# Optimization experiments

Hardware: AMD Instinct MI355X
Metric: run time of the kernel (lower is better)

Reference implementation:

```python
import jax, jax.numpy as jnp
from jax import lax
import numpy as np

TWO_PI = 2.0 * np.pi

# ---- batched real-amplitude statevector simulator (RY/CNOT only -> real state) ----

def _init_state(batch, n):
    s = jnp.zeros((batch, 2 ** n), dtype=jnp.float32).at[:, 0].set(1.0)
    return s.reshape((batch,) + (2,) * n)

def _ry(state, wire, theta, n):
    # state: (B, 2,...,2); theta: scalar or (B,)
    ax = wire + 1
    h = theta * 0.5
    c = jnp.reshape(jnp.cos(h), (-1,) + (1,) * (n - 1))
    s = jnp.reshape(jnp.sin(h), (-1,) + (1,) * (n - 1))
    s0 = lax.index_in_dim(state, 0, ax, keepdims=False)
    s1 = lax.index_in_dim(state, 1, ax, keepdims=False)
    return jnp.stack([c * s0 - s * s1, s * s0 + c * s1], axis=ax)

def _cnot(state, ctrl, tgt):
    axc, axt = ctrl + 1, tgt + 1
    s0 = lax.index_in_dim(state, 0, axc, keepdims=True)
    s1 = lax.index_in_dim(state, 1, axc, keepdims=True)
    return jnp.concatenate([s0, jnp.flip(s1, axis=axt)], axis=axc)

def _expz(state, wire, n):
    sgn = jnp.reshape(jnp.array([1.0, -1.0], state.dtype),
                      (1,) * (wire + 1) + (2,) + (1,) * (n - wire - 1))
    return jnp.sum(state * state * sgn, axis=tuple(range(1, n + 1)))

# gate lists: ('ry', theta_index, wire) or ('cx', control, target)
EDGE_OPS = [('ry',0,0),('ry',1,1),('cx',0,1),('ry',2,2),('ry',3,3),('cx',3,2),
            ('ry',4,4),('ry',5,5),('cx',4,5),('ry',6,6),('ry',7,7),('cx',7,6),
            ('ry',8,1),('ry',9,2),('cx',1,2),('ry',10,5),('ry',11,6),('cx',6,5),
            ('ry',12,2),('ry',13,5),('cx',2,5),('ry',14,5)]

NODE_OPS = [('ry',0,0),('ry',1,1),('cx',0,1),('ry',2,2),('ry',3,3),('cx',3,2),
            ('ry',4,4),('ry',5,5),('cx',4,5),('ry',6,6),('ry',7,7),('cx',7,6),
            ('ry',8,8),('ry',9,9),('cx',8,9),('ry',10,10),('ry',11,11),('cx',11,10),
            ('ry',12,1),('ry',13,2),('cx',1,2),('ry',14,5),('ry',15,6),('cx',6,5),
            ('ry',16,9),('ry',17,10),('cx',10,9),('ry',18,2),('ry',19,5),('cx',2,5),
            ('ry',20,5),('ry',21,9),('cx',5,9),('ry',22,4)]

def _circuit(angles, theta, ops, n, meas_wire):
    st = _init_state(angles.shape[0], n)
    for i in range(n):  # input encoding RYs, per-sample angles
        st = _ry(st, i, angles[:, i], n)
    for op in ops:
        if op[0] == 'ry':
            st = _ry(st, op[2], theta[op[1]], n)
        else:
            st = _cnot(st, op[1], op[2])
    return _expz(st, meas_wire, n)

# ---- GNN pieces ----

def _edge_net(H, Ri, Ro, theta):
    bo = Ro.T @ H                      # [E,4]
    bi = Ri.T @ H                      # [E,4]
    B = jnp.concatenate([bo, bi], axis=1)  # [E,8]
    return (1.0 - _circuit(B, theta, EDGE_OPS, 8, 5)) * 0.5

def _node_net(H, e, Ri, Ro, theta):
    bo = Ro.T @ H                      # [E,4]
    bi = Ri.T @ H                      # [E,4]
    mi = (Ri * e[None, :]) @ bo        # [N,4]
    mo = (Ro * e[None, :]) @ bi        # [N,4]
    M = jnp.concatenate([mi, mo, H], axis=1)  # [N,12]
    return jnp.pi * (1.0 - _circuit(M, theta, NODE_OPS, 12, 9))

def _gnn(X, Ri, Ro, W_in, b_in, theta_edge, theta_node, n_iters=2):
    H = jnp.concatenate([jax.nn.sigmoid(X @ W_in + b_in) * TWO_PI, X], axis=1)  # [N,4]
    e = _edge_net(H, Ri, Ro, theta_edge)
    for _ in range(n_iters):
        h = _node_net(H, e, Ri, Ro, theta_node)   # [N]
        H = jnp.concatenate([h[:, None], X], axis=1)
        e = _edge_net(H, Ri, Ro, theta_edge)
    return e


def setup_inputs() -> dict:
    key = jax.random.key(0)
    ks = jax.random.split(key, 6)
    N, E = 2048, 4096
    X = jax.random.normal(ks[0], (N, 3), jnp.float32)
    recv = jax.random.randint(ks[1], (E,), 0, N)
    send = jax.random.randint(ks[2], (E,), 0, N)
    cols = jnp.arange(E)
    Ri = jnp.zeros((N, E), jnp.float32).at[recv, cols].set(1.0)
    Ro = jnp.zeros((N, E), jnp.float32).at[send, cols].set(1.0)
    W_in = jax.random.normal(ks[3], (3, 1), jnp.float32)
    b_in = jnp.zeros((1,), jnp.float32)
    theta_edge = jax.random.uniform(ks[4], (15,), jnp.float32, 0.0, TWO_PI)
    theta_node = jax.random.uniform(ks[5], (23,), jnp.float32, 0.0, TWO_PI)
    return {'X': X, 'Ri': Ri, 'Ro': Ro, 'W_in': W_in, 'b_in': b_in,
            'theta_edge': theta_edge, 'theta_node': theta_node}


def reference(X, Ri, Ro, W_in, b_in, theta_edge, theta_node):
    return _gnn(X, Ri, Ro, W_in, b_in, theta_edge, theta_node, n_iters=2)
```

## Files before the change

kernel.cpp:

```cpp
#include <hip/hip_runtime.h>
#include <math.h>

#define N_NODES 2048
#define N_EDGES 4096
#define PI_F 3.14159265358979323846f
#define TWO_PI_F 6.28318530717958647692f

#define NBLK 256
#define NTHR 256
#define NSCAN (NBLK * NTHR)
#define TOT4 (N_NODES * N_EDGES / 4)

__device__ __forceinline__ float agent_load(const float* p) {
    return __hip_atomic_load(p, __ATOMIC_RELAXED, __HIP_MEMORY_SCOPE_AGENT);
}
__device__ __forceinline__ int agent_load_i(const int* p) {
    return __hip_atomic_load(p, __ATOMIC_RELAXED, __HIP_MEMORY_SCOPE_AGENT);
}
__device__ __forceinline__ void agent_store_i(int* p, int v) {
    __hip_atomic_store(p, v, __ATOMIC_RELAXED, __HIP_MEMORY_SCOPE_AGENT);
}
__device__ __forceinline__ void spin_ge(const int* p, int v) {
    while (__hip_atomic_load(p, __ATOMIC_RELAXED, __HIP_MEMORY_SCOPE_AGENT) < v)
        __builtin_amdgcn_s_sleep(2);
    asm volatile("" ::: "memory");
}


template<int M>
__device__ __forceinline__ void ry16(float* a, float c, float s) {
#pragma unroll
    for (int i = 0; i < 16; ++i)
        if (!(i & M)) {
            int j = i | M;
            float x0 = a[i], x1 = a[j];
            a[i] = c * x0 - s * x1;
            a[j] = s * x0 + c * x1;
        }
}
template<int MC, int MT>
__device__ __forceinline__ void cx16(float* a) {
#pragma unroll
    for (int i = 0; i < 16; ++i)
        if ((i & MC) && !(i & MT)) {
            int j = i | MT;
            float t = a[i]; a[i] = a[j]; a[j] = t;
        }
}

template<bool BTYPE>
__device__ __forceinline__ void sub16(const float* ic, const float* is,
                                      const float* thc, const float* ths,
                                      float& z, float& x) {
    float a[16];
    a[0] = ic[3]; a[1] = is[3];
#pragma unroll
    for (int i = 0; i < 2; ++i) { a[i | 2] = a[i] * is[2]; a[i] *= ic[2]; }
#pragma unroll
    for (int i = 0; i < 4; ++i) { a[i | 4] = a[i] * is[1]; a[i] *= ic[1]; }
#pragma unroll
    for (int i = 0; i < 8; ++i) { a[i | 8] = a[i] * is[0]; a[i] *= ic[0]; }
    ry16<8>(a, thc[0], ths[0]);
    ry16<4>(a, thc[1], ths[1]);
    cx16<8, 4>(a);
    ry16<2>(a, thc[2], ths[2]);
    ry16<1>(a, thc[3], ths[3]);
    cx16<1, 2>(a);
    ry16<4>(a, thc[4], ths[4]);
    ry16<2>(a, thc[5], ths[5]);
    if (BTYPE) { cx16<2, 4>(a); ry16<4>(a, thc[6], ths[6]); }
    else       { cx16<4, 2>(a); ry16<2>(a, thc[6], ths[6]); }
    const int m = BTYPE ? 4 : 2;
    z = 0.f; x = 0.f;
#pragma unroll
    for (int i = 0; i < 16; ++i) z += (i & m) ? -a[i] * a[i] : a[i] * a[i];
    if (BTYPE) {
#pragma unroll
        for (int i = 0; i < 16; ++i) if (!(i & 4)) x += a[i] * a[i | 4];
        x *= 2.f;
    }
}

__device__ __forceinline__ float node_update(
        const float* M, float& chh, float& shh,
        const float* cxv, const float* sxv,
        const float* tnC, const float* tnS, float C20, float S20) {
    float zB9, dmy;
    {
        float ic[4] = {chh, cxv[0], cxv[1], cxv[2]};
        float is[4] = {shh, sxv[0], sxv[1], sxv[2]};
        float thc[7] = {tnC[8],tnC[9],tnC[10],tnC[11],tnC[16],tnC[17],tnC[21]};
        float ths[7] = {tnS[8],tnS[9],tnS[10],tnS[11],tnS[16],tnS[17],tnS[21]};
        sub16<true>(ic, is, thc, ths, zB9, dmy);
    }
    float mC[8], mS[8];
#pragma unroll
    for (int k = 0; k < 8; ++k) __sincosf(0.5f * M[k], &mS[k], &mC[k]);
    float zA1, zA2, xA2;
    {
        float thc[7] = {tnC[0],tnC[1],tnC[2],tnC[3],tnC[12],tnC[13],tnC[18]};
        float ths[7] = {tnS[0],tnS[1],tnS[2],tnS[3],tnS[12],tnS[13],tnS[18]};
        sub16<false>(&mC[0], &mS[0], thc, ths, zA1, dmy);
    }
    {
        float thc[7] = {tnC[4],tnC[5],tnC[6],tnC[7],tnC[14],tnC[15],tnC[19]};
        float ths[7] = {tnS[4],tnS[5],tnS[6],tnS[7],tnS[14],tnS[15],tnS[19]};
        sub16<true>(&mC[4], &mS[4], thc, ths, zA2, xA2);
    }
    float p9 = (C20*zA1*zA2 - S20*xA2) * zB9;
    float h = PI_F * (1.f - p9);
    __sincosf(0.5f*h, &shh, &chh);
    return h;
}

__device__ __forceinline__ void scatter8(float ev, const float4& Hs, const float4& Hr,
                                         int si, int ri,
                                         float* __restrict__ macc, int* __restrict__ arr) {
    atomicAdd(&macc[ri*8+0], ev*Hs.x); atomicAdd(&macc[ri*8+1], ev*Hs.y);
    atomicAdd(&macc[ri*8+2], ev*Hs.z); atomicAdd(&macc[ri*8+3], ev*Hs.w);
    atomicAdd(&macc[si*8+4], ev*Hr.x); atomicAdd(&macc[si*8+5], ev*Hr.y);
    atomicAdd(&macc[si*8+6], ev*Hr.z); atomicAdd(&macc[si*8+7], ev*Hr.w);
    asm volatile("s_waitcnt vmcnt(0)" ::: "memory");
    atomicAdd(&arr[ri], 1); atomicAdd(&arr[si], 1);
}

__global__ __launch_bounds__(256) void k_fused(
        const float* __restrict__ X, const float* __restrict__ Ri,
        const float* __restrict__ Ro, const float* __restrict__ W,
        const float* __restrict__ b, const float* __restrict__ te,
        const float* __restrict__ tn,
        int* __restrict__ send, int* __restrict__ recv,
        float* __restrict__ maccA, float* __restrict__ maccB,
        int* __restrict__ arrA, int* __restrict__ arrB,
        int* __restrict__ deg, int* __restrict__ sdone,
        float* __restrict__ out) {
    __shared__ float s_teC[16], s_teS[16], s_tnC[24], s_tnS[24];
    int blk = blockIdx.x, tid = threadIdx.x;
    bool edge_blk = (blk < 64);

    if (edge_blk) {
        if (tid < 14) {
            float s, c; __sincosf(0.5f * te[tid], &s, &c);
            s_teC[tid] = c; s_teS[tid] = s;
        } else if (tid == 14) {
            float s, c; __sincosf(te[14], &s, &c);
            s_teC[14] = c; s_teS[14] = s;
        } else if (tid < 15 + 22) {
            int k = tid - 15; float s, c;
            if (k == 20) __sincosf(tn[20], &s, &c);
            else         __sincosf(0.5f * tn[k], &s, &c);
            s_tnC[k] = c; s_tnS[k] = s;
        }
    }

    {
        int gid = blk * NTHR + tid;
        const float4* Ri4 = (const float4*)Ri;
        const float4* Ro4 = (const float4*)Ro;
#pragma unroll 1
        for (int t0 = gid; t0 < TOT4; t0 += 8 * NSCAN) {
            float4 vi[8], vo[8];
#pragma unroll
            for (int u = 0; u < 8; ++u) {
                int t = t0 + u * NSCAN;
                vi[u] = Ri4[t]; vo[u] = Ro4[t];
            }
#pragma unroll
            for (int u = 0; u < 8; ++u) {
                int t = t0 + u * NSCAN;
                int base = t * 4;
                int row = base >> 12;
                int e   = base & (N_EDGES - 1);
                int cnt = 0;
                if (vi[u].x != 0.f) { agent_store_i(recv+e+0, row+1); ++cnt; }
                if (vi[u].y != 0.f) { agent_store_i(recv+e+1, row+1); ++cnt; }
                if (vi[u].z != 0.f) { agent_store_i(recv+e+2, row+1); ++cnt; }
                if (vi[u].w != 0.f) { agent_store_i(recv+e+3, row+1); ++cnt; }
                if (vo[u].x != 0.f) { agent_store_i(send+e+0, row+1); ++cnt; }
                if (vo[u].y != 0.f) { agent_store_i(send+e+1, row+1); ++cnt; }
                if (vo[u].z != 0.f) { agent_store_i(send+e+2, row+1); ++cnt; }
                if (vo[u].w != 0.f) { agent_store_i(send+e+3, row+1); ++cnt; }
                if (cnt) atomicAdd(&deg[row], cnt);
            }
        }
        asm volatile("s_waitcnt vmcnt(0)" ::: "memory");
        __syncthreads();
        if (tid == 0) atomicAdd(sdone, 1);
    }
    if (!edge_blk || tid >= 64) return;

    int e = blk * 64 + tid;

    int si, ri;
    {
        int v;
        while ((v = agent_load_i(send + e)) == 0) __builtin_amdgcn_s_sleep(1);
        si = v - 1;
        while ((v = agent_load_i(recv + e)) == 0) __builtin_amdgcn_s_sleep(1);
        ri = v - 1;
        asm volatile("" ::: "memory");
    }

    float xs0 = X[si*3+0], xs1 = X[si*3+1], xs2 = X[si*3+2];
    float xr0 = X[ri*3+0], xr1 = X[ri*3+1], xr2 = X[ri*3+2];
    float w0 = W[0], w1 = W[1], w2 = W[2], bb = b[0];
    float hs = TWO_PI_F / (1.f + __expf(-(xs0*w0 + xs1*w1 + xs2*w2 + bb)));
    float hr = TWO_PI_F / (1.f + __expf(-(xr0*w0 + xr1*w1 + xr2*w2 + bb)));
    float chs, shs, chr, shr, cxs[3], sxs[3], cxr[3], sxr[3];
    __sincosf(0.5f*hs,  &shs,    &chs);
    __sincosf(0.5f*xs0, &sxs[0], &cxs[0]);
    __sincosf(0.5f*xs1, &sxs[1], &cxs[1]);
    __sincosf(0.5f*xs2, &sxs[2], &cxs[2]);
    __sincosf(0.5f*hr,  &shr,    &chr);
    __sincosf(0.5f*xr0, &sxr[0], &cxr[0]);
    __sincosf(0.5f*xr1, &sxr[1], &cxr[1]);
    __sincosf(0.5f*xr2, &sxr[2], &cxr[2]);
    float C14 = s_teC[14], S14 = s_teS[14];
    float C20 = s_tnC[20], S20 = s_tnS[20];

    float zA, zB, xB, dmy;
    {
        float ic[4] = {chs, cxs[0], cxs[1], cxs[2]};
        float is[4] = {shs, sxs[0], sxs[1], sxs[2]};
        float thc[7] = {s_teC[0],s_teC[1],s_teC[2],s_teC[3],s_teC[8],s_teC[9],s_teC[12]};
        float ths[7] = {s_teS[0],s_teS[1],s_teS[2],s_teS[3],s_teS[8],s_teS[9],s_teS[12]};
        sub16<false>(ic, is, thc, ths, zA, dmy);
    }
    {
        float ic[4] = {chr, cxr[0], cxr[1], cxr[2]};
        float is[4] = {shr, sxr[0], sxr[1], sxr[2]};
        float thc[7] = {s_teC[4],s_teC[5],s_teC[6],s_teC[7],s_teC[10],s_teC[11],s_teC[13]};
        float ths[7] = {s_teS[4],s_teS[5],s_teS[6],s_teS[7],s_teS[10],s_teS[11],s_teS[13]};
        sub16<true>(ic, is, thc, ths, zB, xB);
    }
    float ev = 0.5f*(1.f - (C14*zA*zB - S14*xB));
    scatter8(ev, make_float4(hs, xs0, xs1, xs2),
                 make_float4(hr, xr0, xr1, xr2), si, ri, maccA, arrA);

    spin_ge(sdone, NBLK);
    int dgs = agent_load_i(deg + si);
    int dgr = agent_load_i(deg + ri);

#pragma unroll
    for (int it = 0; it < 2; ++it) {
        const float* mc_ = it ? maccB : maccA;
        const int*   ar  = it ? arrB  : arrA;
        while (agent_load_i(ar + si) < dgs || agent_load_i(ar + ri) < dgr)
            __builtin_amdgcn_s_sleep(1);
        asm volatile("" ::: "memory");
        float Ms[8], Mr[8];
#pragma unroll
        for (int k = 0; k < 8; ++k) Ms[k] = agent_load(mc_ + si*8 + k);
#pragma unroll
        for (int k = 0; k < 8; ++k) Mr[k] = agent_load(mc_ + ri*8 + k);
        hs = node_update(Ms, chs, shs, cxs, sxs, s_tnC, s_tnS, C20, S20);
        hr = node_update(Mr, chr, shr, cxr, sxr, s_tnC, s_tnS, C20, S20);
        {
            float ic[4] = {chs, cxs[0], cxs[1], cxs[2]};
            float is[4] = {shs, sxs[0], sxs[1], sxs[2]};
            float thc[7] = {s_teC[0],s_teC[1],s_teC[2],s_teC[3],s_teC[8],s_teC[9],s_teC[12]};
            float ths[7] = {s_teS[0],s_teS[1],s_teS[2],s_teS[3],s_teS[8],s_teS[9],s_teS[12]};
            sub16<false>(ic, is, thc, ths, zA, dmy);
        }
        {
            float ic[4] = {chr, cxr[0], cxr[1], cxr[2]};
            float is[4] = {shr, sxr[0], sxr[1], sxr[2]};
            float thc[7] = {s_teC[4],s_teC[5],s_teC[6],s_teC[7],s_teC[10],s_teC[11],s_teC[13]};
            float ths[7] = {s_teS[4],s_teS[5],s_teS[6],s_teS[7],s_teS[10],s_teS[11],s_teS[13]};
            sub16<true>(ic, is, thc, ths, zB, xB);
        }
        ev = 0.5f*(1.f - (C14*zA*zB - S14*xB));
        if (it == 0) {
            scatter8(ev, make_float4(hs, xs0, xs1, xs2),
                         make_float4(hr, xr0, xr1, xr2), si, ri, maccB, arrB);
        } else {
            out[e] = ev;
        }
    }
}

extern "C" void kernel_launch(void* const* d_in, const int* in_sizes, int n_in,
                              void* d_out, int out_size, void* d_ws, size_t ws_size,
                              hipStream_t stream) {
    const float* X  = (const float*)d_in[0];
    const float* Ri = (const float*)d_in[1];
    const float* Ro = (const float*)d_in[2];
    const float* W  = (const float*)d_in[3];
    const float* b  = (const float*)d_in[4];
    const float* te = (const float*)d_in[5];
    const float* tn = (const float*)d_in[6];
    float* out = (float*)d_out;

    int*   send  = (int*)d_ws;
    int*   recv  = send + N_EDGES;
    float* maccA = (float*)(recv + N_EDGES);
    float* maccB = maccA + N_NODES * 8;
    int*   arrA  = (int*)(maccB + N_NODES * 8);
    int*   arrB  = arrA + N_NODES;
    int*   deg   = arrB + N_NODES;
    int*   sdone = deg + N_NODES;
    size_t zbytes = (size_t)(2*N_EDGES + 2*N_NODES*8 + 3*N_NODES + 16) * 4;

    hipMemsetAsync((void*)send, 0, zbytes, stream);
    k_fused<<<NBLK, NTHR, 0, stream>>>(X, Ri, Ro, W, b, te, tn,
                                       send, recv, maccA, maccB,
                                       arrA, arrB, deg, sdone, out);
}
```

Baseline: 128.7 us.

## Split dense scan into separate kernel and drop inter-block spin flags

```diff
diff --git a/kernel.cpp b/kernel.cpp
--- a/kernel.cpp
+++ b/kernel.cpp
@@ -6,9 +6,9 @@
 #define PI_F 3.14159265358979323846f
 #define TWO_PI_F 6.28318530717958647692f
 
-#define NBLK 256
-#define NTHR 256
-#define NSCAN (NBLK * NTHR)
+#define SBLK 256
+#define STHR 256
+#define NSCAN (SBLK * STHR)
 #define TOT4 (N_NODES * N_EDGES / 4)
 
 __device__ __forceinline__ float agent_load(const float* p) {
@@ -16,14 +16,6 @@
 }
 __device__ __forceinline__ int agent_load_i(const int* p) {
     return __hip_atomic_load(p, __ATOMIC_RELAXED, __HIP_MEMORY_SCOPE_AGENT);
-}
-__device__ __forceinline__ void agent_store_i(int* p, int v) {
-    __hip_atomic_store(p, v, __ATOMIC_RELAXED, __HIP_MEMORY_SCOPE_AGENT);
-}
-__device__ __forceinline__ void spin_ge(const int* p, int v) {
-    while (__hip_atomic_load(p, __ATOMIC_RELAXED, __HIP_MEMORY_SCOPE_AGENT) < v)
-        __builtin_amdgcn_s_sleep(2);
-    asm volatile("" ::: "memory");
 }
 
 
@@ -81,125 +73,82 @@
     }
 }
 
-__device__ __forceinline__ float node_update(
-        const float* M, float& chh, float& shh,
-        const float* cxv, const float* sxv,
-        const float* tnC, const float* tnS, float C20, float S20) {
-    float zB9, dmy;
-    {
-        float ic[4] = {chh, cxv[0], cxv[1], cxv[2]};
-        float is[4] = {shh, sxv[0], sxv[1], sxv[2]};
-        float thc[7] = {tnC[8],tnC[9],tnC[10],tnC[11],tnC[16],tnC[17],tnC[21]};
-        float ths[7] = {tnS[8],tnS[9],tnS[10],tnS[11],tnS[16],tnS[17],tnS[21]};
-        sub16<true>(ic, is, thc, ths, zB9, dmy);
-    }
-    float mC[8], mS[8];
-#pragma unroll
-    for (int k = 0; k < 8; ++k) __sincosf(0.5f * M[k], &mS[k], &mC[k]);
-    float zA1, zA2, xA2;
-    {
-        float thc[7] = {tnC[0],tnC[1],tnC[2],tnC[3],tnC[12],tnC[13],tnC[18]};
-        float ths[7] = {tnS[0],tnS[1],tnS[2],tnS[3],tnS[12],tnS[13],tnS[18]};
-        sub16<false>(&mC[0], &mS[0], thc, ths, zA1, dmy);
-    }
-    {
-        float thc[7] = {tnC[4],tnC[5],tnC[6],tnC[7],tnC[14],tnC[15],tnC[19]};
-        float ths[7] = {tnS[4],tnS[5],tnS[6],tnS[7],tnS[14],tnS[15],tnS[19]};
-        sub16<true>(&mC[4], &mS[4], thc, ths, zA2, xA2);
-    }
-    float p9 = (C20*zA1*zA2 - S20*xA2) * zB9;
-    float h = PI_F * (1.f - p9);
-    __sincosf(0.5f*h, &shh, &chh);
-    return h;
-}
-
-__device__ __forceinline__ void scatter8(float ev, const float4& Hs, const float4& Hr,
+__global__ __launch_bounds__(256) void k_scan(
+        const float* __restrict__ Ri, const float* __restrict__ Ro,
+        int* __restrict__ send, int* __restrict__ recv, int* __restrict__ deg) {
+    int gid = blockIdx.x * STHR + threadIdx.x;
+    const float4* Ri4 = (const float4*)Ri;
+    const float4* Ro4 = (const float4*)Ro;
+#pragma unroll 1
+    for (int t0 = gid; t0 < TOT4; t0 += 8 * NSCAN) {
+        float4 vi[8], vo[8];
+#pragma unroll
+        for (int u = 0; u < 8; ++u) {
+            int t = t0 + u * NSCAN;
+            vi[u] = Ri4[t]; vo[u] = Ro4[t];
+        }
+#pragma unroll
+        for (int u = 0; u < 8; ++u) {
+            int t = t0 + u * NSCAN;
+            int base = t * 4;
+            int row = base >> 12;
+            int e   = base & (N_EDGES - 1);
+            int cnt = 0;
+            if (vi[u].x != 0.f) { recv[e+0] = row; ++cnt; }
+            if (vi[u].y != 0.f) { recv[e+1] = row; ++cnt; }
+            if (vi[u].z != 0.f) { recv[e+2] = row; ++cnt; }
+            if (vi[u].w != 0.f) { recv[e+3] = row; ++cnt; }
+            if (vo[u].x != 0.f) { send[e+0] = row; ++cnt; }
+            if (vo[u].y != 0.f) { send[e+1] = row; ++cnt; }
+            if (vo[u].z != 0.f) { send[e+2] = row; ++cnt; }
+            if (vo[u].w != 0.f) { send[e+3] = row; ++cnt; }
+            if (cnt) atomicAdd(&deg[row], cnt);
+        }
+    }
+}
+
+__device__ __forceinline__ void scatter8(float ev, float hs, float hr,
+                                         float xs0, float xs1, float xs2,
+                                         float xr0, float xr1, float xr2,
                                          int si, int ri,
                                          float* __restrict__ macc, int* __restrict__ arr) {
-    atomicAdd(&macc[ri*8+0], ev*Hs.x); atomicAdd(&macc[ri*8+1], ev*Hs.y);
-    atomicAdd(&macc[ri*8+2], ev*Hs.z); atomicAdd(&macc[ri*8+3], ev*Hs.w);
-    atomicAdd(&macc[si*8+4], ev*Hr.x); atomicAdd(&macc[si*8+5], ev*Hr.y);
-    atomicAdd(&macc[si*8+6], ev*Hr.z); atomicAdd(&macc[si*8+7], ev*Hr.w);
+    atomicAdd(&macc[ri*8+0], ev*hs);  atomicAdd(&macc[ri*8+1], ev*xs0);
+    atomicAdd(&macc[ri*8+2], ev*xs1); atomicAdd(&macc[ri*8+3], ev*xs2);
+    atomicAdd(&macc[si*8+4], ev*hr);  atomicAdd(&macc[si*8+5], ev*xr0);
+    atomicAdd(&macc[si*8+6], ev*xr1); atomicAdd(&macc[si*8+7], ev*xr2);
     asm volatile("s_waitcnt vmcnt(0)" ::: "memory");
     atomicAdd(&arr[ri], 1); atomicAdd(&arr[si], 1);
 }
 
-__global__ __launch_bounds__(256) void k_fused(
-        const float* __restrict__ X, const float* __restrict__ Ri,
-        const float* __restrict__ Ro, const float* __restrict__ W,
+__global__ __launch_bounds__(64) void k_mega(
+        const float* __restrict__ X, const float* __restrict__ W,
         const float* __restrict__ b, const float* __restrict__ te,
         const float* __restrict__ tn,
-        int* __restrict__ send, int* __restrict__ recv,
+        const int* __restrict__ send, const int* __restrict__ recv,
+        const int* __restrict__ deg,
         float* __restrict__ maccA, float* __restrict__ maccB,
         int* __restrict__ arrA, int* __restrict__ arrB,
-        int* __restrict__ deg, int* __restrict__ sdone,
         float* __restrict__ out) {
     __shared__ float s_teC[16], s_teS[16], s_tnC[24], s_tnS[24];
-    int blk = blockIdx.x, tid = threadIdx.x;
-    bool edge_blk = (blk < 64);
-
-    if (edge_blk) {
-        if (tid < 14) {
-            float s, c; __sincosf(0.5f * te[tid], &s, &c);
-            s_teC[tid] = c; s_teS[tid] = s;
-        } else if (tid == 14) {
-            float s, c; __sincosf(te[14], &s, &c);
-            s_teC[14] = c; s_teS[14] = s;
-        } else if (tid < 15 + 22) {
-            int k = tid - 15; float s, c;
-            if (k == 20) __sincosf(tn[20], &s, &c);
-            else         __sincosf(0.5f * tn[k], &s, &c);
-            s_tnC[k] = c; s_tnS[k] = s;
-        }
-    }
-
-    {
-        int gid = blk * NTHR + tid;
-        const float4* Ri4 = (const float4*)Ri;
-        const float4* Ro4 = (const float4*)Ro;
-#pragma unroll 1
-        for (int t0 = gid; t0 < TOT4; t0 += 8 * NSCAN) {
-            float4 vi[8], vo[8];
-#pragma unroll
-            for (int u = 0; u < 8; ++u) {
-                int t = t0 + u * NSCAN;
-                vi[u] = Ri4[t]; vo[u] = Ro4[t];
-            }
-#pragma unroll
-            for (int u = 0; u < 8; ++u) {
-                int t = t0 + u * NSCAN;
-                int base = t * 4;
-                int row = base >> 12;
-                int e   = base & (N_EDGES - 1);
-                int cnt = 0;
-                if (vi[u].x != 0.f) { agent_store_i(recv+e+0, row+1); ++cnt; }
-                if (vi[u].y != 0.f) { agent_store_i(recv+e+1, row+1); ++cnt; }
-                if (vi[u].z != 0.f) { agent_store_i(recv+e+2, row+1); ++cnt; }
-                if (vi[u].w != 0.f) { agent_store_i(recv+e+3, row+1); ++cnt; }
-                if (vo[u].x != 0.f) { agent_store_i(send+e+0, row+1); ++cnt; }
-                if (vo[u].y != 0.f) { agent_store_i(send+e+1, row+1); ++cnt; }
-                if (vo[u].z != 0.f) { agent_store_i(send+e+2, row+1); ++cnt; }
-                if (vo[u].w != 0.f) { agent_store_i(send+e+3, row+1); ++cnt; }
-                if (cnt) atomicAdd(&deg[row], cnt);
-            }
-        }
-        asm volatile("s_waitcnt vmcnt(0)" ::: "memory");
-        __syncthreads();
-        if (tid == 0) atomicAdd(sdone, 1);
-    }
-    if (!edge_blk || tid >= 64) return;
-
-    int e = blk * 64 + tid;
-
-    int si, ri;
-    {
-        int v;
-        while ((v = agent_load_i(send + e)) == 0) __builtin_amdgcn_s_sleep(1);
-        si = v - 1;
-        while ((v = agent_load_i(recv + e)) == 0) __builtin_amdgcn_s_sleep(1);
-        ri = v - 1;
-        asm volatile("" ::: "memory");
-    }
+    int tid = threadIdx.x;
+
+    if (tid < 14) {
+        float s, c; __sincosf(0.5f * te[tid], &s, &c);
+        s_teC[tid] = c; s_teS[tid] = s;
+    } else if (tid == 14) {
+        float s, c; __sincosf(te[14], &s, &c);
+        s_teC[14] = c; s_teS[14] = s;
+    } else if (tid < 15 + 22) {
+        int k = tid - 15; float s, c;
+        if (k == 20) __sincosf(tn[20], &s, &c);
+        else         __sincosf(0.5f * tn[k], &s, &c);
+        s_tnC[k] = c; s_tnS[k] = s;
+    }
+    __syncthreads();
+
+    int e = blockIdx.x * 64 + tid;
+    int si = send[e], ri = recv[e];
+    int dgs = deg[si], dgr = deg[ri];
 
     float xs0 = X[si*3+0], xs1 = X[si*3+1], xs2 = X[si*3+2];
     float xr0 = X[ri*3+0], xr1 = X[ri*3+1], xr2 = X[ri*3+2];
@@ -234,27 +183,50 @@
         sub16<true>(ic, is, thc, ths, zB, xB);
     }
     float ev = 0.5f*(1.f - (C14*zA*zB - S14*xB));
-    scatter8(ev, make_float4(hs, xs0, xs1, xs2),
-                 make_float4(hr, xr0, xr1, xr2), si, ri, maccA, arrA);
-
-    spin_ge(sdone, NBLK);
-    int dgs = agent_load_i(deg + si);
-    int dgr = agent_load_i(deg + ri);
+    scatter8(ev, hs, hr, xs0, xs1, xs2, xr0, xr1, xr2, si, ri, maccA, arrA);
 
 #pragma unroll
     for (int it = 0; it < 2; ++it) {
-        const float* mc_ = it ? maccB : maccA;
-        const int*   ar  = it ? arrB  : arrA;
-        while (agent_load_i(ar + si) < dgs || agent_load_i(ar + ri) < dgr)
-            __builtin_amdgcn_s_sleep(1);
+        float* mc_ = it ? maccB : maccA;
+        int*   ar  = it ? arrB  : arrA;
+        float zB9s, zB9r;
+        {
+            float thc[7] = {s_tnC[8],s_tnC[9],s_tnC[10],s_tnC[11],s_tnC[16],s_tnC[17],s_tnC[21]};
+            float ths[7] = {s_tnS[8],s_tnS[9],s_tnS[10],s_tnS[11],s_tnS[16],s_tnS[17],s_tnS[21]};
+            float ic[4] = {chs, cxs[0], cxs[1], cxs[2]};
+            float is[4] = {shs, sxs[0], sxs[1], sxs[2]};
+            sub16<true>(ic, is, thc, ths, zB9s, dmy);
+            float ic2[4] = {chr, cxr[0], cxr[1], cxr[2]};
+            float is2[4] = {shr, sxr[0], sxr[1], sxr[2]};
+            sub16<true>(ic2, is2, thc, ths, zB9r, dmy);
+        }
+        while (agent_load_i(ar + si) < dgs || agent_load_i(ar + ri) < dgr) {}
         asm volatile("" ::: "memory");
         float Ms[8], Mr[8];
 #pragma unroll
         for (int k = 0; k < 8; ++k) Ms[k] = agent_load(mc_ + si*8 + k);
 #pragma unroll
         for (int k = 0; k < 8; ++k) Mr[k] = agent_load(mc_ + ri*8 + k);
-        hs = node_update(Ms, chs, shs, cxs, sxs, s_tnC, s_tnS, C20, S20);
-        hr = node_update(Mr, chr, shr, cxr, sxr, s_tnC, s_tnS, C20, S20);
+
+        float mCs[8], mSs[8], mCr[8], mSr[8];
+#pragma unroll
+        for (int k = 0; k < 8; ++k) __sincosf(0.5f*Ms[k], &mSs[k], &mCs[k]);
+#pragma unroll
+        for (int k = 0; k < 8; ++k) __sincosf(0.5f*Mr[k], &mSr[k], &mCr[k]);
+        float thcA1[7] = {s_tnC[0],s_tnC[1],s_tnC[2],s_tnC[3],s_tnC[12],s_tnC[13],s_tnC[18]};
+        float thsA1[7] = {s_tnS[0],s_tnS[1],s_tnS[2],s_tnS[3],s_tnS[12],s_tnS[13],s_tnS[18]};
+        float thcA2[7] = {s_tnC[4],s_tnC[5],s_tnC[6],s_tnC[7],s_tnC[14],s_tnC[15],s_tnC[19]};
+        float thsA2[7] = {s_tnS[4],s_tnS[5],s_tnS[6],s_tnS[7],s_tnS[14],s_tnS[15],s_tnS[19]};
+        float zA1, zA2, xA2;
+        sub16<false>(&mCs[0], &mSs[0], thcA1, thsA1, zA1, dmy);
+        sub16<true >(&mCs[4], &mSs[4], thcA2, thsA2, zA2, xA2);
+        hs = PI_F * (1.f - (C20*zA1*zA2 - S20*xA2) * zB9s);
+        __sincosf(0.5f*hs, &shs, &chs);
+        sub16<false>(&mCr[0], &mSr[0], thcA1, thsA1, zA1, dmy);
+        sub16<true >(&mCr[4], &mSr[4], thcA2, thsA2, zA2, xA2);
+        hr = PI_F * (1.f - (C20*zA1*zA2 - S20*xA2) * zB9r);
+        __sincosf(0.5f*hr, &shr, &chr);
+
         {
             float ic[4] = {chs, cxs[0], cxs[1], cxs[2]};
             float is[4] = {shs, sxs[0], sxs[1], sxs[2]};
@@ -271,8 +243,7 @@
         }
         ev = 0.5f*(1.f - (C14*zA*zB - S14*xB));
         if (it == 0) {
-            scatter8(ev, make_float4(hs, xs0, xs1, xs2),
-                         make_float4(hr, xr0, xr1, xr2), si, ri, maccB, arrB);
+            scatter8(ev, hs, hr, xs0, xs1, xs2, xr0, xr1, xr2, si, ri, maccB, arrB);
         } else {
             out[e] = ev;
         }
@@ -298,11 +269,10 @@
     int*   arrA  = (int*)(maccB + N_NODES * 8);
     int*   arrB  = arrA + N_NODES;
     int*   deg   = arrB + N_NODES;
-    int*   sdone = deg + N_NODES;
-    size_t zbytes = (size_t)(2*N_EDGES + 2*N_NODES*8 + 3*N_NODES + 16) * 4;
-
-    hipMemsetAsync((void*)send, 0, zbytes, stream);
-    k_fused<<<NBLK, NTHR, 0, stream>>>(X, Ri, Ro, W, b, te, tn,
-                                       send, recv, maccA, maccB,
-                                       arrA, arrB, deg, sdone, out);
-}
+    size_t zbytes = (size_t)(2*N_NODES*8 + 3*N_NODES) * 4;
+
+    hipMemsetAsync((void*)maccA, 0, zbytes, stream);
+    k_scan<<<SBLK, STHR, 0, stream>>>(Ri, Ro, send, recv, deg);
+    k_mega<<<64, 64, 0, stream>>>(X, W, b, te, tn, send, recv, deg,
+                                  maccA, maccB, arrA, arrB, out);
+}
```

Result: no change. 129.5 us (+0.6%).
